# Optimization experiments

Hardware: AMD Instinct MI355X
Metric: run time of the kernel (lower is better)

The kernel has to match this reference:

```python
import jax, jax.numpy as jnp
import numpy as np

D, NH, L, P, FF = 256, 8, 3, 4, 1024
DH = D // NH
EPS = 1e-5

def _ln(x, g, b):
    m = jnp.mean(x, axis=-1, keepdims=True)
    v = jnp.mean((x - m) ** 2, axis=-1, keepdims=True)
    return (x - m) * jax.lax.rsqrt(v + EPS) * g + b

def _bilinear(value, loc, Hl, Wl):
    # value: [B,NH,Nl,DH]; loc (x,y) in [0,1]: [B,N,NH,P,2]; grid_sample align_corners=False, zero padding
    B, N = loc.shape[0], loc.shape[1]
    x = loc[..., 0] * Wl - 0.5
    y = loc[..., 1] * Hl - 0.5
    x0 = jnp.floor(x)
    y0 = jnp.floor(y)
    lx, ly = x - x0, y - y0
    x0 = x0.astype(jnp.int32)
    y0 = y0.astype(jnp.int32)

    def gather(xi, yi):
        valid = ((xi >= 0) & (xi < Wl) & (yi >= 0) & (yi < Hl)).astype(value.dtype)
        idx = jnp.clip(yi, 0, Hl - 1) * Wl + jnp.clip(xi, 0, Wl - 1)  # [B,N,NH,P]
        idx = idx.transpose(0, 2, 1, 3).reshape(B, NH, N * P, 1)
        v = jnp.take_along_axis(value, idx, axis=2)  # [B,NH,N*P,DH]
        v = v.reshape(B, NH, N, P, DH).transpose(0, 2, 1, 3, 4)  # [B,N,NH,P,DH]
        return v * valid[..., None]

    v00 = gather(x0, y0)
    v01 = gather(x0 + 1, y0)
    v10 = gather(x0, y0 + 1)
    v11 = gather(x0 + 1, y0 + 1)
    return (v00 * ((1 - lx) * (1 - ly))[..., None] + v01 * (lx * (1 - ly))[..., None]
            + v10 * ((1 - lx) * ly)[..., None] + v11 * (lx * ly)[..., None])

def _forward(query, p3, p4, p5, Wv, bv, Woff, boff, Wattn, battn, Wref, bref, Wo, bo,
             W1, b1, W2, b2, g1, be1, g2, be2, shapes):
    B, N, _ = query.shape
    off = (query @ Woff + boff).reshape(B, N, NH, L, P, 2)
    aw = jax.nn.softmax((query @ Wattn + battn).reshape(B, N, NH, L * P), axis=-1).reshape(B, N, NH, L, P)
    ref = jax.nn.sigmoid(query @ Wref + bref)[:, :, None, None, :]  # [B,N,1,1,2]
    out = jnp.zeros((B, N, NH, DH), query.dtype)
    for l, (feat, (Hl, Wl)) in enumerate(zip((p3, p4, p5), shapes)):
        val = (feat @ Wv + bv).reshape(B, Hl * Wl, NH, DH).transpose(0, 2, 1, 3)  # [B,NH,Nl,DH]
        loc = ref + off[:, :, :, l] / jnp.array([Wl, Hl], query.dtype)  # offsets normalized by (W,H)
        samp = _bilinear(val, loc, Hl, Wl)  # [B,N,NH,P,DH]
        out = out + jnp.einsum('bnhp,bnhpd->bnhd', aw[:, :, :, l], samp)
    attn_out = out.reshape(B, N, D) @ Wo + bo
    q = _ln(query + attn_out, g1, be1)  # residual + norm1 (dropout=eval identity)
    ffn = jax.nn.gelu(q @ W1 + b1, approximate=False) @ W2 + b2
    return _ln(q + ffn, g2, be2)

def setup_inputs():
    key = jax.random.key(0)
    ks = jax.random.split(key, 12)
    B = 4
    H3, W3, H4, W4, H5, W5 = 100, 100, 50, 50, 25, 25
    N = H3 * W3 + H4 * W4 + H5 * W5
    s = 0.02
    f32 = jnp.float32
    return dict(
        query=jax.random.normal(ks[0], (B, N, D), f32),
        p3=jax.random.normal(ks[1], (B, H3 * W3, D), f32),
        p4=jax.random.normal(ks[2], (B, H4 * W4, D), f32),
        p5=jax.random.normal(ks[3], (B, H5 * W5, D), f32),
        Wv=jax.random.normal(ks[4], (D, D), f32) * s, bv=jnp.zeros((D,), f32),
        Woff=jax.random.normal(ks[5], (D, NH * L * P * 2), f32) * s, boff=jnp.zeros((NH * L * P * 2,), f32),
        Wattn=jax.random.normal(ks[6], (D, NH * L * P), f32) * s, battn=jnp.zeros((NH * L * P,), f32),
        Wref=jax.random.normal(ks[7], (D, 2), f32) * s, bref=jnp.zeros((2,), f32),
        Wo=jax.random.normal(ks[8], (D, D), f32) * s, bo=jnp.zeros((D,), f32),
        W1=jax.random.normal(ks[9], (D, FF), f32) * s, b1=jnp.zeros((FF,), f32),
        W2=jax.random.normal(ks[10], (FF, D), f32) * s, b2=jnp.zeros((D,), f32),
        g1=jnp.ones((D,), f32), be1=jnp.zeros((D,), f32),
        g2=jnp.ones((D,), f32), be2=jnp.zeros((D,), f32),
        H3=H3, W3=W3, H4=H4, W4=W4, H5=H5, W5=W5,
    )

def reference(query, p3, p4, p5, Wv, bv, Woff, boff, Wattn, battn, Wref, bref, Wo, bo,
              W1, b1, W2, b2, g1, be1, g2, be2, H3, W3, H4, W4, H5, W5):
    return _forward(query, p3, p4, p5, Wv, bv, Woff, boff, Wattn, battn, Wref, bref, Wo, bo,
                    W1, b1, W2, b2, g1, be1, g2, be2, ((H3, W3), (H4, W4), (H5, W5)))
```

## Files before the change

### kernel.cpp

```cpp
#include <hip/hip_runtime.h>
#include <math.h>

#define BQ    4
#define NTOT  13125
#define DD    256
#define NHH   8
#define FFD   1024
#define EPSLN 1e-5f
#define MROWS (BQ * NTOT)
#define MPAD  52736
#define NCHUNK 26250
#define NCHUNK_PAD 26368

typedef __bf16 bf16_t;
typedef bf16_t bf16x8 __attribute__((ext_vector_type(8)));
typedef float floatx4 __attribute__((ext_vector_type(4)));

__device__ __forceinline__ unsigned short f2bf(float f) {
    unsigned u = __float_as_uint(f);
    return (unsigned short)((u + 0x7FFFu + ((u >> 16) & 1u)) >> 16);
}
__device__ __forceinline__ float bf2f(unsigned short h) {
    return __uint_as_float(((unsigned)h) << 16);
}

typedef const __attribute__((address_space(1))) unsigned int* gptr_t;
typedef __attribute__((address_space(3))) unsigned int* lptr_t;
__device__ __forceinline__ void gld16(const void* g, void* l) {
    __builtin_amdgcn_global_load_lds((gptr_t)g, (lptr_t)l, 16, 0, 0);
}

enum { EPI_F32 = 0, EPI_BF16 = 1, EPI_GELU = 2, EPI_VALSEG = 3 };

__device__ __forceinline__ int val_row(int gm) {
    if (gm < 40064) {
        if (gm >= 40000) return -1;
        int b = gm / 10000; int nl = gm - b * 10000;
        return b * NTOT + nl;
    } else if (gm < 50176) {
        int r = gm - 40064;
        if (r >= 10000) return -1;
        int b = r / 2500; int nl = r - b * 2500;
        return b * NTOT + 10000 + nl;
    } else {
        int r = gm - 50176;
        if (r >= 2500) return -1;
        int b = r / 625; int nl = r - b * 625;
        return b * NTOT + 12500 + nl;
    }
}

template <int EPI, typename OutT>
__launch_bounds__(256)
__global__ void mm_k(const unsigned short* __restrict__ A,
                     const unsigned short* __restrict__ Bt,
                     const float* __restrict__ bias, OutT* __restrict__ C,
                     int M, int K, int Nout, int ldc, int Mstore) {
    __shared__ __align__(16) unsigned short As[128 * 32];
    __shared__ __align__(16) unsigned short Bs[128 * 32];

    const int tid = threadIdx.x;
    const int m0 = blockIdx.x * 128;
    const int n0 = blockIdx.y * 128;
    const int w = tid >> 6, lane = tid & 63;
    const int q = lane >> 4, l15 = lane & 15;
    const int wm = (w & 1) * 64, wn = (w >> 1) * 64;

    const int sr = tid >> 2;
    const int sk = (tid & 3) * 8;

    const unsigned short* Ag = A + (size_t)(m0 + sr) * K + sk;
    const unsigned short* Bg = Bt + (size_t)(n0 + sr) * K + sk;
    char* AsB = (char*)As;
    char* BsB = (char*)Bs;

    floatx4 acc[4][4];
#pragma unroll
    for (int t = 0; t < 4; t++)
#pragma unroll
        for (int u = 0; u < 4; u++) {
            floatx4 z = {0.f, 0.f, 0.f, 0.f};
            acc[t][u] = z;
        }

    for (int k0 = 0; k0 < K; k0 += 32) {
        gld16(Ag + k0, AsB + tid * 16);
        gld16(Ag + (size_t)64 * K + k0, AsB + 4096 + tid * 16);
        gld16(Bg + k0, BsB + tid * 16);
        gld16(Bg + (size_t)64 * K + k0, BsB + 4096 + tid * 16);
        __syncthreads();

        bf16x8 af[4], bfr[4];
#pragma unroll
        for (int t = 0; t < 4; t++)
            af[t] = *reinterpret_cast<const bf16x8*>(&As[(wm + t * 16 + l15) * 32 + q * 8]);
#pragma unroll
        for (int u = 0; u < 4; u++)
            bfr[u] = *reinterpret_cast<const bf16x8*>(&Bs[(wn + u * 16 + l15) * 32 + q * 8]);
#pragma unroll
        for (int t = 0; t < 4; t++)
#pragma unroll
            for (int u = 0; u < 4; u++)
                acc[t][u] = __builtin_amdgcn_mfma_f32_16x16x32_bf16(af[t], bfr[u], acc[t][u], 0, 0, 0);
        __syncthreads();
    }

    float bias_v[4];
#pragma unroll
    for (int u = 0; u < 4; u++) {
        int gn = n0 + wn + u * 16 + l15;
        bias_v[u] = (gn < Nout) ? bias[gn] : 0.f;
    }

#pragma unroll
    for (int t = 0; t < 4; t++) {
#pragma unroll
        for (int r = 0; r < 4; r++) {
            int gm = m0 + wm + t * 16 + q * 4 + r;
            int orow = gm;
            if (EPI == EPI_VALSEG) orow = val_row(gm);
#pragma unroll
            for (int u = 0; u < 4; u++) {
                int gn = n0 + wn + u * 16 + l15;
                if (gn >= Nout) continue;
                float v = acc[t][u][r] + bias_v[u];
                if (EPI == EPI_GELU) {
                    v = 0.5f * v * (1.f + erff(v * 0.70710678118f));
                    if (gm < Mstore) {
                        float ov = (gm < M) ? v : 0.f;
                        ((unsigned short*)C)[(size_t)gm * ldc + gn] = f2bf(ov);
                    }
                } else if (EPI == EPI_VALSEG) {
                    if (orow >= 0)
                        ((unsigned short*)C)[(size_t)orow * ldc + gn] = f2bf(v);
                } else if (EPI == EPI_BF16) {
                    if (gm < M) ((unsigned short*)C)[(size_t)gm * ldc + gn] = f2bf(v);
                } else {
                    if (gm < M) ((float*)C)[(size_t)gm * ldc + gn] = v;
                }
            }
        }
    }
}

#define QELEMS   13500416
#define F3ELEMS  10256384
#define F4ELEMS   2588672
#define TOTELEMS 27000832

__launch_bounds__(256)
__global__ void cast_acts_k(const float* __restrict__ query, const float* __restrict__ p3,
                            const float* __restrict__ p4, const float* __restrict__ p5,
                            unsigned short* __restrict__ qbf, unsigned short* __restrict__ featsb) {
    int idx4 = (blockIdx.x * 256 + threadIdx.x) * 4;
    if (idx4 >= TOTELEMS) return;
    const float* src; unsigned short* dst; int local, real;
    if (idx4 < QELEMS) {
        src = query; dst = qbf; local = idx4; real = 13440000;
    } else {
        int j = idx4 - QELEMS;
        if (j < F3ELEMS)              { src = p3; dst = featsb;                    local = j;            real = 10240000; }
        else if (j < F3ELEMS + F4ELEMS){ src = p4; dst = featsb + F3ELEMS;         local = j - F3ELEMS;  real = 2560000; }
        else                          { src = p5; dst = featsb + F3ELEMS + F4ELEMS; local = j - F3ELEMS - F4ELEMS; real = 640000; }
    }
    float4 v = make_float4(0.f, 0.f, 0.f, 0.f);
    if (local < real) v = *(const float4*)&src[local];
    ushort4 o;
    o.x = f2bf(v.x); o.y = f2bf(v.y); o.z = f2bf(v.z); o.w = f2bf(v.w);
    *(ushort4*)&dst[local] = o;
}

#define WTQ_E   98304
#define WTV_E   (WTQ_E + 65536)
#define WTO_E   (WTV_E + 65536)
#define WT1_E   (WTO_E + 262144)
#define WT2_E   (WT1_E + 262144)
#define PREP_TOT (WT2_E + 384)

__launch_bounds__(256)
__global__ void prep_w_k(const float* __restrict__ Woff, const float* __restrict__ Wattn,
                         const float* __restrict__ Wv, const float* __restrict__ Wo,
                         const float* __restrict__ W1, const float* __restrict__ W2,
                         const float* __restrict__ boff, const float* __restrict__ battn,
                         unsigned short* __restrict__ warena, float* __restrict__ biasq) {
    int i = blockIdx.x * 256 + threadIdx.x;
    if (i >= PREP_TOT) return;
    if (i >= WT2_E) {
        int t = i - WT2_E;
        biasq[t] = (t < 192) ? boff[t] : (t < 288 ? battn[t - 192] : 0.f);
        return;
    }
    float v;
    if (i < WTQ_E) {
        int n = i >> 8, k = i & 255;
        v = (n < 192) ? Woff[k * 192 + n] : (n < 288 ? Wattn[k * 96 + (n - 192)] : 0.f);
    } else if (i < WTV_E) {
        int j = i - WTQ_E; int n = j >> 8, k = j & 255;
        v = Wv[k * 256 + n];
    } else if (i < WTO_E) {
        int j = i - WTV_E; int n = j >> 8, k = j & 255;
        v = Wo[k * 256 + n];
    } else if (i < WT1_E) {
        int j = i - WTO_E; int n = j >> 8, k = j & 255;
        v = W1[k * 1024 + n];
    } else {
        int j = i - WT1_E; int n = j >> 10, k = j & 1023;
        v = W2[k * 256 + n];
    }
    warena[i] = f2bf(v);
}

__launch_bounds__(256)
__global__ void ref_k(const float* __restrict__ Q, const float* __restrict__ Wref,
                      const float* __restrict__ bref, float* __restrict__ refb) {
    int wid = threadIdx.x >> 6;
    int lane = threadIdx.x & 63;
    int row = blockIdx.x * 4 + wid;
    if (row >= MROWS) return;
    float4 qv = *(const float4*)&Q[(size_t)row * DD + lane * 4];
    float4 w01 = *(const float4*)&Wref[lane * 8];
    float4 w23 = *(const float4*)&Wref[lane * 8 + 4];
    float s0 = qv.x * w01.x + qv.y * w01.z + qv.z * w23.x + qv.w * w23.z;
    float s1 = qv.x * w01.y + qv.y * w01.w + qv.z * w23.y + qv.w * w23.w;
#pragma unroll
    for (int m = 32; m >= 1; m >>= 1) {
        s0 += __shfl_xor(s0, m);
        s1 += __shfl_xor(s1, m);
    }
    if (lane == 0) {
        float v0 = s0 + bref[0], v1 = s1 + bref[1];
        refb[(size_t)row * 2 + 0] = 1.f / (1.f + expf(-v0));
        refb[(size_t)row * 2 + 1] = 1.f / (1.f + expf(-v1));
    }
}

__launch_bounds__(256)
__global__ void softmax12_k(const float* __restrict__ projb, unsigned short* __restrict__ aw) {
    int rh = blockIdx.x * 256 + threadIdx.x;
    if (rh >= MROWS * NHH) return;
    int bn = rh >> 3, h = rh & 7;
    const float* p = projb + (size_t)bn * 288 + 192 + h * 12;
    float v[12], mx = -1e30f;
#pragma unroll
    for (int i = 0; i < 12; i++) { v[i] = p[i]; mx = fmaxf(mx, v[i]); }
    float s = 0.f;
#pragma unroll
    for (int i = 0; i < 12; i++) { v[i] = expf(v[i] - mx); s += v[i]; }
    float inv = 1.f / s;
    unsigned short* o = aw + (size_t)rh * 12;
#pragma unroll
    for (int i = 0; i < 12; i++) o[i] = f2bf(v[i] * inv);
}

__launch_bounds__(64)
__global__ void sample_k(const unsigned short* __restrict__ val, const float* __restrict__ off,
                         const unsigned short* __restrict__ aw, const float* __restrict__ refb,
                         unsigned short* __restrict__ out) {
    const int bn = blockIdx.x;
    const int b = bn / NTOT;
    const int tid = threadIdx.x;
    __shared__ float sw[96][4];
    __shared__ int sidx[96][4];

    float rx = refb[(size_t)bn * 2 + 0];
    float ry = refb[(size_t)bn * 2 + 1];
    for (int s0 = tid; s0 < 96; s0 += 64) {
        const int lp = s0 % 12;
        const int l = lp >> 2;
        int Hl, Wl, loff;
        if (l == 0)      { Hl = 100; Wl = 100; loff = 0; }
        else if (l == 1) { Hl = 50;  Wl = 50;  loff = 10000; }
        else             { Hl = 25;  Wl = 25;  loff = 12500; }
        float ox = off[(size_t)bn * 288 + s0 * 2 + 0];
        float oy = off[(size_t)bn * 288 + s0 * 2 + 1];
        float a  = bf2f(aw[(size_t)bn * 96 + s0]);
        float x = rx * (float)Wl + ox - 0.5f;
        float y = ry * (float)Hl + oy - 0.5f;
        x = fminf(fmaxf(x, -1e4f), 1e4f);
        y = fminf(fmaxf(y, -1e4f), 1e4f);
        float x0f = floorf(x), y0f = floorf(y);
        float lx = x - x0f, ly = y - y0f;
        int x0 = (int)x0f, y0 = (int)y0f;
#pragma unroll
        for (int c = 0; c < 4; c++) {
            int xi = x0 + (c & 1);
            int yi = y0 + (c >> 1);
            bool ok = (xi >= 0) && (xi < Wl) && (yi >= 0) && (yi < Hl);
            int xc = min(max(xi, 0), Wl - 1);
            int yc = min(max(yi, 0), Hl - 1);
            sidx[s0][c] = b * NTOT + loff + yc * Wl + xc;
            float wgt = ((c & 1) ? lx : 1.f - lx) * ((c >> 1) ? ly : 1.f - ly);
            sw[s0][c] = ok ? a * wgt : 0.f;
        }
    }
    __syncthreads();

    const int h = tid >> 3;
    const int dq = (tid & 7) * 4;
    const unsigned short* vb = val + h * 32 + dq;
    float a0 = 0.f, a1 = 0.f, a2 = 0.f, a3 = 0.f;
#pragma unroll
    for (int lp = 0; lp < 12; lp++) {
        int s = h * 12 + lp;
#pragma unroll
        for (int c = 0; c < 4; c++) {
            float wgt = sw[s][c];
            uint2 u = *(const uint2*)(vb + (size_t)sidx[s][c] * DD);
            a0 += wgt * __uint_as_float(u.x << 16);
            a1 += wgt * __uint_as_float(u.x & 0xFFFF0000u);
            a2 += wgt * __uint_as_float(u.y << 16);
            a3 += wgt * __uint_as_float(u.y & 0xFFFF0000u);
        }
    }
    uint2 ov;
    ov.x = (unsigned)f2bf(a0) | ((unsigned)f2bf(a1) << 16);
    ov.y = (unsigned)f2bf(a2) | ((unsigned)f2bf(a3) << 16);
    *(uint2*)(out + (size_t)bn * DD + h * 32 + dq) = ov;
}

template <typename RT, int WBF>
__launch_bounds__(256)
__global__ void addln_k(const float* __restrict__ a, const RT* __restrict__ r,
                        const float* __restrict__ g, const float* __restrict__ be,
                        float* __restrict__ out, unsigned short* __restrict__ outb, int nrows) {
    int wid = threadIdx.x >> 6;
    int lane = threadIdx.x & 63;
    int row = blockIdx.x * 4 + wid;
    if (row >= nrows) return;
    float4 xa = *(const float4*)&a[(size_t)row * DD + lane * 4];
    float x0, x1, x2, x3;
    if (sizeof(RT) == 2) {
        ushort4 rv = *(const ushort4*)((const unsigned short*)r + (size_t)row * DD + lane * 4);
        x0 = xa.x + bf2f(rv.x); x1 = xa.y + bf2f(rv.y);
        x2 = xa.z + bf2f(rv.z); x3 = xa.w + bf2f(rv.w);
    } else {
        float4 rv = *(const float4*)((const float*)r + (size_t)row * DD + lane * 4);
        x0 = xa.x + rv.x; x1 = xa.y + rv.y; x2 = xa.z + rv.z; x3 = xa.w + rv.w;
    }
    float s = x0 + x1 + x2 + x3;
    float sq = x0 * x0 + x1 * x1 + x2 * x2 + x3 * x3;
#pragma unroll
    for (int m = 32; m >= 1; m >>= 1) {
        s += __shfl_xor(s, m);
        sq += __shfl_xor(sq, m);
    }
    float mean = s * (1.f / DD);
    float var = sq * (1.f / DD) - mean * mean;
    float rs = rsqrtf(var + EPSLN);
    float4 gg = *(const float4*)&g[lane * 4];
    float4 bb = *(const float4*)&be[lane * 4];
    float4 o;
    o.x = (x0 - mean) * rs * gg.x + bb.x;
    o.y = (x1 - mean) * rs * gg.y + bb.y;
    o.z = (x2 - mean) * rs * gg.z + bb.z;
    o.w = (x3 - mean) * rs * gg.w + bb.w;
    *(float4*)&out[(size_t)row * DD + lane * 4] = o;
    if (WBF) {
        ushort4 ob;
        ob.x = f2bf(o.x); ob.y = f2bf(o.y); ob.z = f2bf(o.z); ob.w = f2bf(o.w);
        *(ushort4*)&outb[(size_t)row * DD + lane * 4] = ob;
    }
}

extern "C" void kernel_launch(void* const* d_in, const int* in_sizes, int n_in,
                              void* d_out, int out_size, void* d_ws, size_t ws_size,
                              hipStream_t stream) {
    const float* query = (const float*)d_in[0];
    const float* p3    = (const float*)d_in[1];
    const float* p4    = (const float*)d_in[2];
    const float* p5    = (const float*)d_in[3];
    const float* Wv    = (const float*)d_in[4];
    const float* bv    = (const float*)d_in[5];
    const float* Woff  = (const float*)d_in[6];
    const float* boff  = (const float*)d_in[7];
    const float* Wattn = (const float*)d_in[8];
    const float* battn = (const float*)d_in[9];
    const float* Wref  = (const float*)d_in[10];
    const float* bref  = (const float*)d_in[11];
    const float* Wo    = (const float*)d_in[12];
    const float* bo    = (const float*)d_in[13];
    const float* W1    = (const float*)d_in[14];
    const float* b1    = (const float*)d_in[15];
    const float* W2    = (const float*)d_in[16];
    const float* b2    = (const float*)d_in[17];
    const float* g1    = (const float*)d_in[18];
    const float* be1   = (const float*)d_in[19];
    const float* g2    = (const float*)d_in[20];
    const float* be2   = (const float*)d_in[21];
    float* outp = (float*)d_out;

    char* wsb = (char*)d_ws;
    unsigned short* qbf    = (unsigned short*)(wsb + 0);
    float*          projb  = (float*)(wsb + 27000832);
    unsigned short* awb    = (unsigned short*)(wsb + 87752704);
    float*          refb   = (float*)(wsb + 97832704);
    unsigned short* featsb = (unsigned short*)(wsb + 98252704);
    unsigned short* valb   = (unsigned short*)(wsb + 125253536);
    unsigned short* sampb  = (unsigned short*)(wsb + 152133536);
    unsigned short* warena = (unsigned short*)(wsb + 179068832);
    float*          biasq  = (float*)(wsb + 180576160);
    unsigned short* attnbf = valb;
    float*          qf32   = projb;
    unsigned short* hidb   = awb;
    float*          ffnb   = (float*)(wsb + 141752320);

    unsigned short* Wtq = warena;
    unsigned short* Wtv = warena + WTQ_E;
    unsigned short* Wto = warena + WTV_E;
    unsigned short* Wt1 = warena + WTO_E;
    unsigned short* Wt2 = warena + WT1_E;

    cast_acts_k<<<dim3(TOTELEMS / 4 / 256), 256, 0, stream>>>(query, p3, p4, p5, qbf, featsb);
    prep_w_k<<<dim3((PREP_TOT + 255) / 256), 256, 0, stream>>>(
        Woff, Wattn, Wv, Wo, W1, W2, boff, battn, warena, biasq);
    ref_k<<<dim3((MROWS + 3) / 4), 256, 0, stream>>>(query, Wref, bref, refb);
    mm_k<EPI_F32, float><<<dim3(MPAD / 128, 3), 256, 0, stream>>>(
        qbf, Wtq, biasq, projb, MROWS, 256, 288, 288, 0);
    softmax12_k<<<dim3((MROWS * NHH + 255) / 256), 256, 0, stream>>>(projb, awb);
    mm_k<EPI_VALSEG, unsigned short><<<dim3(MPAD / 128, 2), 256, 0, stream>>>(
        featsb, Wtv, bv, valb, 0, 256, 256, 256, 0);
    sample_k<<<dim3(MROWS), 64, 0, stream>>>(valb, projb, awb, refb, sampb);
    mm_k<EPI_BF16, unsigned short><<<dim3(52608 / 128, 2), 256, 0, stream>>>(
        sampb, Wto, bo, attnbf, MROWS, 256, 256, 256, 0);
    addln_k<unsigned short, 1><<<dim3(MROWS / 4), 256, 0, stream>>>(
        query, attnbf, g1, be1, qf32, qbf, MROWS);
    for (int c = 0; c < 2; c++) {
        const unsigned short* qc = qbf + (size_t)c * NCHUNK * DD;
        mm_k<EPI_GELU, unsigned short><<<dim3(NCHUNK_PAD / 128, FFD / 128), 256, 0, stream>>>(
            qc, Wt1, b1, hidb, NCHUNK, 256, FFD, FFD, NCHUNK_PAD);
        mm_k<EPI_F32, float><<<dim3(NCHUNK_PAD / 128, 2), 256, 0, stream>>>(
            hidb, Wt2, b2, ffnb, NCHUNK, FFD, 256, 256, 0);
        addln_k<float, 0><<<dim3((NCHUNK + 3) / 4), 256, 0, stream>>>(
            qf32 + (size_t)c * NCHUNK * DD, ffnb, g2, be2,
            outp + (size_t)c * NCHUNK * DD, (unsigned short*)nullptr, NCHUNK);
    }
}
```

Baseline: 675.8 us.

## Fuse residual LayerNorm into output and FFN2 GEMMs, fold ref projection into Q GEMM

Adds a gemmln_k kernel that computes a 64x256 GEMM tile and applies bias, residual add and LayerNorm in its epilogue. It is used for the attention output projection (with LN1) and for FFN2 (with LN2), replacing the separate addln kernels and their intermediate round trips through global memory. The reference-point projection is folded into the query projection GEMM as two extra columns, and the row stride widens to 320; ref_k is removed and the sigmoid moves into sample_k, which now handles two query rows per block with packed weight/offset entries in LDS. The FFN is no longer split into two chunks. The LN2 residual is now read from the bf16 query copy instead of fp32, which lowers accuracy slightly. The new GEMM has no double-buffering.

New measurement: 598.6 us. -11.4%, faster.

```diff
diff --git a/kernel.cpp b/kernel.cpp
--- a/kernel.cpp
+++ b/kernel.cpp
@@ -9,8 +9,6 @@
 #define EPSLN 1e-5f
 #define MROWS (BQ * NTOT)
 #define MPAD  52736
-#define NCHUNK 26250
-#define NCHUNK_PAD 26368
 
 typedef __bf16 bf16_t;
 typedef bf16_t bf16x8 __attribute__((ext_vector_type(8)));
@@ -30,7 +28,7 @@
     __builtin_amdgcn_global_load_lds((gptr_t)g, (lptr_t)l, 16, 0, 0);
 }
 
-enum { EPI_F32 = 0, EPI_BF16 = 1, EPI_GELU = 2, EPI_VALSEG = 3 };
+enum { EPI_F32 = 0, EPI_GELU = 2, EPI_VALSEG = 3 };
 
 __device__ __forceinline__ int val_row(int gm) {
     if (gm < 40064) {
@@ -133,10 +131,145 @@
                 } else if (EPI == EPI_VALSEG) {
                     if (orow >= 0)
                         ((unsigned short*)C)[(size_t)orow * ldc + gn] = f2bf(v);
-                } else if (EPI == EPI_BF16) {
-                    if (gm < M) ((unsigned short*)C)[(size_t)gm * ldc + gn] = f2bf(v);
                 } else {
                     if (gm < M) ((float*)C)[(size_t)gm * ldc + gn] = v;
+                }
+            }
+        }
+    }
+}
+
+template <typename RT, typename OT>
+__launch_bounds__(256)
+__global__ void gemmln_k(const unsigned short* __restrict__ A,
+                         const unsigned short* __restrict__ Bt,
+                         const float* __restrict__ bias, const RT* __restrict__ res,
+                         const float* __restrict__ g, const float* __restrict__ be,
+                         OT* __restrict__ out, int M, int K) {
+    __shared__ __align__(16) unsigned short As[64 * 32];
+    __shared__ __align__(16) unsigned short Bs[256 * 32];
+
+    const int tid = threadIdx.x;
+    const int m0 = blockIdx.x * 64;
+    const int w = tid >> 6, lane = tid & 63;
+    const int q = lane >> 4, l15 = lane & 15;
+    const int wn = w * 64;
+
+    const int sr = tid >> 2;
+    const int sk = (tid & 3) * 8;
+    const unsigned short* Ag = A + (size_t)(m0 + sr) * K + sk;
+    const unsigned short* Bg = Bt + (size_t)sr * K + sk;
+    char* AsB = (char*)As;
+    char* BsB = (char*)Bs;
+
+    floatx4 acc[4][4];
+#pragma unroll
+    for (int t = 0; t < 4; t++)
+#pragma unroll
+        for (int u = 0; u < 4; u++) {
+            floatx4 z = {0.f, 0.f, 0.f, 0.f};
+            acc[t][u] = z;
+        }
+
+    for (int k0 = 0; k0 < K; k0 += 32) {
+        gld16(Ag + k0, AsB + tid * 16);
+#pragma unroll
+        for (int j = 0; j < 4; j++)
+            gld16(Bg + (size_t)j * 64 * K + k0, BsB + j * 4096 + tid * 16);
+        __syncthreads();
+
+        bf16x8 af[4], bfr[4];
+#pragma unroll
+        for (int t = 0; t < 4; t++)
+            af[t] = *reinterpret_cast<const bf16x8*>(&As[(t * 16 + l15) * 32 + q * 8]);
+#pragma unroll
+        for (int u = 0; u < 4; u++)
+            bfr[u] = *reinterpret_cast<const bf16x8*>(&Bs[(wn + u * 16 + l15) * 32 + q * 8]);
+#pragma unroll
+        for (int t = 0; t < 4; t++)
+#pragma unroll
+            for (int u = 0; u < 4; u++)
+                acc[t][u] = __builtin_amdgcn_mfma_f32_16x16x32_bf16(af[t], bfr[u], acc[t][u], 0, 0, 0);
+        __syncthreads();
+    }
+
+    float gg[4], bb[4], bias_v[4];
+#pragma unroll
+    for (int u = 0; u < 4; u++) {
+        int gn = wn + u * 16 + l15;
+        gg[u] = g[gn]; bb[u] = be[gn]; bias_v[u] = bias[gn];
+    }
+
+    float x[4][4][4];
+    float ssum[4][4], ssq[4][4];
+#pragma unroll
+    for (int t = 0; t < 4; t++) {
+#pragma unroll
+        for (int r = 0; r < 4; r++) {
+            int gm = m0 + t * 16 + q * 4 + r;
+            bool valid = gm < M;
+            float s = 0.f, sq = 0.f;
+#pragma unroll
+            for (int u = 0; u < 4; u++) {
+                int gn = wn + u * 16 + l15;
+                float rv = 0.f;
+                if (valid) {
+                    if (sizeof(RT) == 2)
+                        rv = bf2f(((const unsigned short*)res)[(size_t)gm * DD + gn]);
+                    else
+                        rv = ((const float*)res)[(size_t)gm * DD + gn];
+                }
+                float xx = acc[t][u][r] + bias_v[u] + rv;
+                x[t][r][u] = xx;
+                s += xx; sq += xx * xx;
+            }
+            ssum[t][r] = s; ssq[t][r] = sq;
+        }
+    }
+#pragma unroll
+    for (int m = 1; m <= 8; m <<= 1) {
+#pragma unroll
+        for (int t = 0; t < 4; t++)
+#pragma unroll
+            for (int r = 0; r < 4; r++) {
+                ssum[t][r] += __shfl_xor(ssum[t][r], m);
+                ssq[t][r] += __shfl_xor(ssq[t][r], m);
+            }
+    }
+    float* Ls = (float*)As;
+    float* Lq = Ls + 256;
+    if (l15 == 0) {
+#pragma unroll
+        for (int t = 0; t < 4; t++)
+#pragma unroll
+            for (int r = 0; r < 4; r++) {
+                int lr = t * 16 + q * 4 + r;
+                Ls[lr * 4 + w] = ssum[t][r];
+                Lq[lr * 4 + w] = ssq[t][r];
+            }
+    }
+    __syncthreads();
+
+#pragma unroll
+    for (int t = 0; t < 4; t++) {
+#pragma unroll
+        for (int r = 0; r < 4; r++) {
+            int lr = t * 16 + q * 4 + r;
+            int gm = m0 + lr;
+            float tot = Ls[lr * 4 + 0] + Ls[lr * 4 + 1] + Ls[lr * 4 + 2] + Ls[lr * 4 + 3];
+            float totq = Lq[lr * 4 + 0] + Lq[lr * 4 + 1] + Lq[lr * 4 + 2] + Lq[lr * 4 + 3];
+            float mean = tot * (1.f / DD);
+            float var = totq * (1.f / DD) - mean * mean;
+            float rs = rsqrtf(var + EPSLN);
+            if (gm < M) {
+#pragma unroll
+                for (int u = 0; u < 4; u++) {
+                    int gn = wn + u * 16 + l15;
+                    float o = (x[t][r][u] - mean) * rs * gg[u] + bb[u];
+                    if (sizeof(OT) == 2)
+                        ((unsigned short*)out)[(size_t)gm * DD + gn] = f2bf(o);
+                    else
+                        ((float*)out)[(size_t)gm * DD + gn] = o;
                 }
             }
         }
@@ -179,21 +312,24 @@
 
 __launch_bounds__(256)
 __global__ void prep_w_k(const float* __restrict__ Woff, const float* __restrict__ Wattn,
-                         const float* __restrict__ Wv, const float* __restrict__ Wo,
-                         const float* __restrict__ W1, const float* __restrict__ W2,
-                         const float* __restrict__ boff, const float* __restrict__ battn,
+                         const float* __restrict__ Wref, const float* __restrict__ Wv,
+                         const float* __restrict__ Wo, const float* __restrict__ W1,
+                         const float* __restrict__ W2, const float* __restrict__ boff,
+                         const float* __restrict__ battn, const float* __restrict__ bref,
                          unsigned short* __restrict__ warena, float* __restrict__ biasq) {
     int i = blockIdx.x * 256 + threadIdx.x;
     if (i >= PREP_TOT) return;
     if (i >= WT2_E) {
         int t = i - WT2_E;
-        biasq[t] = (t < 192) ? boff[t] : (t < 288 ? battn[t - 192] : 0.f);
+        biasq[t] = (t < 192) ? boff[t] : (t < 288 ? battn[t - 192] : (t < 290 ? bref[t - 288] : 0.f));
         return;
     }
     float v;
     if (i < WTQ_E) {
         int n = i >> 8, k = i & 255;
-        v = (n < 192) ? Woff[k * 192 + n] : (n < 288 ? Wattn[k * 96 + (n - 192)] : 0.f);
+        v = (n < 192) ? Woff[k * 192 + n]
+          : (n < 288) ? Wattn[k * 96 + (n - 192)]
+          : (n < 290) ? Wref[k * 2 + (n - 288)] : 0.f;
     } else if (i < WTV_E) {
         int j = i - WTQ_E; int n = j >> 8, k = j & 255;
         v = Wv[k * 256 + n];
@@ -211,35 +347,11 @@
 }
 
 __launch_bounds__(256)
-__global__ void ref_k(const float* __restrict__ Q, const float* __restrict__ Wref,
-                      const float* __restrict__ bref, float* __restrict__ refb) {
-    int wid = threadIdx.x >> 6;
-    int lane = threadIdx.x & 63;
-    int row = blockIdx.x * 4 + wid;
-    if (row >= MROWS) return;
-    float4 qv = *(const float4*)&Q[(size_t)row * DD + lane * 4];
-    float4 w01 = *(const float4*)&Wref[lane * 8];
-    float4 w23 = *(const float4*)&Wref[lane * 8 + 4];
-    float s0 = qv.x * w01.x + qv.y * w01.z + qv.z * w23.x + qv.w * w23.z;
-    float s1 = qv.x * w01.y + qv.y * w01.w + qv.z * w23.y + qv.w * w23.w;
-#pragma unroll
-    for (int m = 32; m >= 1; m >>= 1) {
-        s0 += __shfl_xor(s0, m);
-        s1 += __shfl_xor(s1, m);
-    }
-    if (lane == 0) {
-        float v0 = s0 + bref[0], v1 = s1 + bref[1];
-        refb[(size_t)row * 2 + 0] = 1.f / (1.f + expf(-v0));
-        refb[(size_t)row * 2 + 1] = 1.f / (1.f + expf(-v1));
-    }
-}
-
-__launch_bounds__(256)
 __global__ void softmax12_k(const float* __restrict__ projb, unsigned short* __restrict__ aw) {
     int rh = blockIdx.x * 256 + threadIdx.x;
     if (rh >= MROWS * NHH) return;
     int bn = rh >> 3, h = rh & 7;
-    const float* p = projb + (size_t)bn * 288 + 192 + h * 12;
+    const float* p = projb + (size_t)bn * 320 + 192 + h * 12;
     float v[12], mx = -1e30f;
 #pragma unroll
     for (int i = 0; i < 12; i++) { v[i] = p[i]; mx = fmaxf(mx, v[i]); }
@@ -252,27 +364,28 @@
     for (int i = 0; i < 12; i++) o[i] = f2bf(v[i] * inv);
 }
 
-__launch_bounds__(64)
-__global__ void sample_k(const unsigned short* __restrict__ val, const float* __restrict__ off,
-                         const unsigned short* __restrict__ aw, const float* __restrict__ refb,
+__launch_bounds__(128)
+__global__ void sample_k(const unsigned short* __restrict__ val, const float* __restrict__ projb,
+                         const unsigned short* __restrict__ aw,
                          unsigned short* __restrict__ out) {
-    const int bn = blockIdx.x;
+    const int wv = threadIdx.x >> 6;
+    const int lane = threadIdx.x & 63;
+    const int bn = blockIdx.x * 2 + wv;
     const int b = bn / NTOT;
-    const int tid = threadIdx.x;
-    __shared__ float sw[96][4];
-    __shared__ int sidx[96][4];
-
-    float rx = refb[(size_t)bn * 2 + 0];
-    float ry = refb[(size_t)bn * 2 + 1];
-    for (int s0 = tid; s0 < 96; s0 += 64) {
+    __shared__ uint2 sc[2][96][4];
+
+    const float* prow = projb + (size_t)bn * 320;
+    float rx = 1.f / (1.f + expf(-prow[288]));
+    float ry = 1.f / (1.f + expf(-prow[289]));
+    for (int s0 = lane; s0 < 96; s0 += 64) {
         const int lp = s0 % 12;
         const int l = lp >> 2;
         int Hl, Wl, loff;
         if (l == 0)      { Hl = 100; Wl = 100; loff = 0; }
         else if (l == 1) { Hl = 50;  Wl = 50;  loff = 10000; }
         else             { Hl = 25;  Wl = 25;  loff = 12500; }
-        float ox = off[(size_t)bn * 288 + s0 * 2 + 0];
-        float oy = off[(size_t)bn * 288 + s0 * 2 + 1];
+        float ox = prow[s0 * 2 + 0];
+        float oy = prow[s0 * 2 + 1];
         float a  = bf2f(aw[(size_t)bn * 96 + s0]);
         float x = rx * (float)Wl + ox - 0.5f;
         float y = ry * (float)Hl + oy - 0.5f;
@@ -288,24 +401,25 @@
             bool ok = (xi >= 0) && (xi < Wl) && (yi >= 0) && (yi < Hl);
             int xc = min(max(xi, 0), Wl - 1);
             int yc = min(max(yi, 0), Hl - 1);
-            sidx[s0][c] = b * NTOT + loff + yc * Wl + xc;
+            int idx = b * NTOT + loff + yc * Wl + xc;
             float wgt = ((c & 1) ? lx : 1.f - lx) * ((c >> 1) ? ly : 1.f - ly);
-            sw[s0][c] = ok ? a * wgt : 0.f;
+            sc[wv][s0][c] = make_uint2(__float_as_uint(ok ? a * wgt : 0.f), (unsigned)(idx * 512));
         }
     }
     __syncthreads();
 
-    const int h = tid >> 3;
-    const int dq = (tid & 7) * 4;
-    const unsigned short* vb = val + h * 32 + dq;
+    const int h = lane >> 3;
+    const int dq = (lane & 7) * 4;
+    const char* vb = (const char*)val + h * 64 + dq * 2;
     float a0 = 0.f, a1 = 0.f, a2 = 0.f, a3 = 0.f;
 #pragma unroll
     for (int lp = 0; lp < 12; lp++) {
         int s = h * 12 + lp;
 #pragma unroll
         for (int c = 0; c < 4; c++) {
-            float wgt = sw[s][c];
-            uint2 u = *(const uint2*)(vb + (size_t)sidx[s][c] * DD);
+            uint2 p = sc[wv][s][c];
+            float wgt = __uint_as_float(p.x);
+            uint2 u = *(const uint2*)(vb + p.y);
             a0 += wgt * __uint_as_float(u.x << 16);
             a1 += wgt * __uint_as_float(u.x & 0xFFFF0000u);
             a2 += wgt * __uint_as_float(u.y << 16);
@@ -316,50 +430,6 @@
     ov.x = (unsigned)f2bf(a0) | ((unsigned)f2bf(a1) << 16);
     ov.y = (unsigned)f2bf(a2) | ((unsigned)f2bf(a3) << 16);
     *(uint2*)(out + (size_t)bn * DD + h * 32 + dq) = ov;
-}
-
-template <typename RT, int WBF>
-__launch_bounds__(256)
-__global__ void addln_k(const float* __restrict__ a, const RT* __restrict__ r,
-                        const float* __restrict__ g, const float* __restrict__ be,
-                        float* __restrict__ out, unsigned short* __restrict__ outb, int nrows) {
-    int wid = threadIdx.x >> 6;
-    int lane = threadIdx.x & 63;
-    int row = blockIdx.x * 4 + wid;
-    if (row >= nrows) return;
-    float4 xa = *(const float4*)&a[(size_t)row * DD + lane * 4];
-    float x0, x1, x2, x3;
-    if (sizeof(RT) == 2) {
-        ushort4 rv = *(const ushort4*)((const unsigned short*)r + (size_t)row * DD + lane * 4);
-        x0 = xa.x + bf2f(rv.x); x1 = xa.y + bf2f(rv.y);
-        x2 = xa.z + bf2f(rv.z); x3 = xa.w + bf2f(rv.w);
-    } else {
-        float4 rv = *(const float4*)((const float*)r + (size_t)row * DD + lane * 4);
-        x0 = xa.x + rv.x; x1 = xa.y + rv.y; x2 = xa.z + rv.z; x3 = xa.w + rv.w;
-    }
-    float s = x0 + x1 + x2 + x3;
-    float sq = x0 * x0 + x1 * x1 + x2 * x2 + x3 * x3;
-#pragma unroll
-    for (int m = 32; m >= 1; m >>= 1) {
-        s += __shfl_xor(s, m);
-        sq += __shfl_xor(sq, m);
-    }
-    float mean = s * (1.f / DD);
-    float var = sq * (1.f / DD) - mean * mean;
-    float rs = rsqrtf(var + EPSLN);
-    float4 gg = *(const float4*)&g[lane * 4];
-    float4 bb = *(const float4*)&be[lane * 4];
-    float4 o;
-    o.x = (x0 - mean) * rs * gg.x + bb.x;
-    o.y = (x1 - mean) * rs * gg.y + bb.y;
-    o.z = (x2 - mean) * rs * gg.z + bb.z;
-    o.w = (x3 - mean) * rs * gg.w + bb.w;
-    *(float4*)&out[(size_t)row * DD + lane * 4] = o;
-    if (WBF) {
-        ushort4 ob;
-        ob.x = f2bf(o.x); ob.y = f2bf(o.y); ob.z = f2bf(o.z); ob.w = f2bf(o.w);
-        *(ushort4*)&outb[(size_t)row * DD + lane * 4] = ob;
-    }
 }
 
 extern "C" void kernel_launch(void* const* d_in, const int* in_sizes, int n_in,
@@ -392,17 +462,13 @@
     char* wsb = (char*)d_ws;
     unsigned short* qbf    = (unsigned short*)(wsb + 0);
     float*          projb  = (float*)(wsb + 27000832);
-    unsigned short* awb    = (unsigned short*)(wsb + 87752704);
-    float*          refb   = (float*)(wsb + 97832704);
-    unsigned short* featsb = (unsigned short*)(wsb + 98252704);
-    unsigned short* valb   = (unsigned short*)(wsb + 125253536);
-    unsigned short* sampb  = (unsigned short*)(wsb + 152133536);
-    unsigned short* warena = (unsigned short*)(wsb + 179068832);
-    float*          biasq  = (float*)(wsb + 180576160);
-    unsigned short* attnbf = valb;
-    float*          qf32   = projb;
-    unsigned short* hidb   = awb;
-    float*          ffnb   = (float*)(wsb + 141752320);
+    unsigned short* awb    = (unsigned short*)(wsb + 94502912);
+    unsigned short* featsb = (unsigned short*)(wsb + 104582912);
+    unsigned short* valb   = (unsigned short*)(wsb + 131583744);
+    unsigned short* sampb  = (unsigned short*)(wsb + 158463744);
+    unsigned short* warena = (unsigned short*)(wsb + 185399296);
+    float*          biasq  = (float*)(wsb + 186906624);
+    unsigned short* hidb   = (unsigned short*)(wsb + 27000832);
 
     unsigned short* Wtq = warena;
     unsigned short* Wtv = warena + WTQ_E;
@@ -412,26 +478,17 @@
 
     cast_acts_k<<<dim3(TOTELEMS / 4 / 256), 256, 0, stream>>>(query, p3, p4, p5, qbf, featsb);
     prep_w_k<<<dim3((PREP_TOT + 255) / 256), 256, 0, stream>>>(
-        Woff, Wattn, Wv, Wo, W1, W2, boff, battn, warena, biasq);
-    ref_k<<<dim3((MROWS + 3) / 4), 256, 0, stream>>>(query, Wref, bref, refb);
+        Woff, Wattn, Wref, Wv, Wo, W1, W2, boff, battn, bref, warena, biasq);
     mm_k<EPI_F32, float><<<dim3(MPAD / 128, 3), 256, 0, stream>>>(
-        qbf, Wtq, biasq, projb, MROWS, 256, 288, 288, 0);
+        qbf, Wtq, biasq, projb, MROWS, 256, 290, 320, 0);
     softmax12_k<<<dim3((MROWS * NHH + 255) / 256), 256, 0, stream>>>(projb, awb);
     mm_k<EPI_VALSEG, unsigned short><<<dim3(MPAD / 128, 2), 256, 0, stream>>>(
         featsb, Wtv, bv, valb, 0, 256, 256, 256, 0);
-    sample_k<<<dim3(MROWS), 64, 0, stream>>>(valb, projb, awb, refb, sampb);
-    mm_k<EPI_BF16, unsigned short><<<dim3(52608 / 128, 2), 256, 0, stream>>>(
-        sampb, Wto, bo, attnbf, MROWS, 256, 256, 256, 0);
-    addln_k<unsigned short, 1><<<dim3(MROWS / 4), 256, 0, stream>>>(
-        query, attnbf, g1, be1, qf32, qbf, MROWS);
-    for (int c = 0; c < 2; c++) {
-        const unsigned short* qc = qbf + (size_t)c * NCHUNK * DD;
-        mm_k<EPI_GELU, unsigned short><<<dim3(NCHUNK_PAD / 128, FFD / 128), 256, 0, stream>>>(
-            qc, Wt1, b1, hidb, NCHUNK, 256, FFD, FFD, NCHUNK_PAD);
-        mm_k<EPI_F32, float><<<dim3(NCHUNK_PAD / 128, 2), 256, 0, stream>>>(
-            hidb, Wt2, b2, ffnb, NCHUNK, FFD, 256, 256, 0);
-        addln_k<float, 0><<<dim3((NCHUNK + 3) / 4), 256, 0, stream>>>(
-            qf32 + (size_t)c * NCHUNK * DD, ffnb, g2, be2,
-            outp + (size_t)c * NCHUNK * DD, (unsigned short*)nullptr, NCHUNK);
-    }
-}
+    sample_k<<<dim3(MROWS / 2), 128, 0, stream>>>(valb, projb, awb, sampb);
+    gemmln_k<float, unsigned short><<<dim3((MROWS + 63) / 64), 256, 0, stream>>>(
+        sampb, Wto, bo, query, g1, be1, qbf, MROWS, 256);
+    mm_k<EPI_GELU, unsigned short><<<dim3(MPAD / 128, FFD / 128), 256, 0, stream>>>(
+        qbf, Wt1, b1, hidb, MROWS, 256, FFD, FFD, MPAD);
+    gemmln_k<unsigned short, float><<<dim3((MROWS + 63) / 64), 256, 0, stream>>>(
+        hidb, Wt2, b2, qbf, g2, be2, outp, MROWS, 1024);
+}
```
